# Performance work log

Hardware: AMD Instinct MI355X
Metric: run time of the kernel (lower is better)

Reference implementation:

```python
import jax, jax.numpy as jnp
import numpy as np

B, IN, H, T = 512, 256, 128, 100

def _build_norm_adj():
    # Hardcoded topology from GraphConvLSTM.build_graph (22 nodes, cliques per sublist)
    adj_list = [[0, 2, 5, 8, 11], [0, 1, 4, 7, 10], [0, 3, 6, 9, 12, 15],
                [9, 14, 17, 19, 21], [9, 13, 16, 18, 20]]
    n = max(max(s) for s in adj_list) + 1  # 22
    A = np.zeros((n, n), dtype=np.float32)
    for s in adj_list:
        for i in range(len(s)):
            for j in range(i + 1, len(s)):
                A[s[i], s[j]] = 1.0
                A[s[j], s[i]] = 1.0
    # DGL GraphConv norm='both': D^{-1/2} A D^{-1/2} (degrees clamped to >=1)
    deg = np.clip(A.sum(axis=1), 1.0, None)
    dinv = 1.0 / np.sqrt(deg)
    return jnp.asarray(dinv[:, None] * A * dinv[None, :])  # (N, N)

A_NORM = _build_norm_adj()
N = A_NORM.shape[0]  # 22

def setup_inputs() -> dict:
    key = jax.random.key(0)
    ks = jax.random.split(key, 11)
    s_in = 1.0 / np.sqrt(IN)
    s_h = 1.0 / np.sqrt(H)
    return {
        "x":     jax.random.normal(ks[0], (B, IN), jnp.float32),
        "wi_w":  jax.random.normal(ks[1], (H, IN), jnp.float32) * s_in,
        "wi_b":  jax.random.normal(ks[2], (H,), jnp.float32) * s_in,
        "wf_w":  jax.random.normal(ks[3], (H, IN), jnp.float32) * s_in,
        "wf_b":  jax.random.normal(ks[4], (H,), jnp.float32) * s_in,
        "wo_w":  jax.random.normal(ks[5], (H, IN), jnp.float32) * s_in,
        "wo_b":  jax.random.normal(ks[6], (H,), jnp.float32) * s_in,
        "wc_w":  jax.random.normal(ks[7], (H, IN), jnp.float32) * s_in,
        "wc_b":  jax.random.normal(ks[8], (H,), jnp.float32) * s_in,
        "gcn_w": jax.random.normal(ks[9], (H, H), jnp.float32) * s_h,
        "gcn_b": jax.random.normal(ks[10], (H,), jnp.float32) * s_h,
    }

def reference(x, wi_w, wi_b, wf_w, wf_b, wo_w, wo_b, wc_w, wc_b, gcn_w, gcn_b):
    # x is fixed across timesteps in the original forward -> project gates once.
    xi = (x @ wi_w.T + wi_b)[:, None, :]  # (B,1,H) broadcast over nodes
    xf = (x @ wf_w.T + wf_b)[:, None, :]
    xo = (x @ wo_w.T + wo_b)[:, None, :]
    xc = (x @ wc_w.T + wc_b)[:, None, :]

    def step(carry, _):
        h, c = carry
        # All four gates share the identical gcn_h(g, h_prev) result.
        msg = jnp.einsum('mn,bnh->bmh', A_NORM, h)  # (B,N,H)
        g = msg @ gcn_w + gcn_b
        i_t = jax.nn.sigmoid(xi + g)
        f_t = jax.nn.sigmoid(xf + g)
        o_t = jax.nn.sigmoid(xo + g)
        c_til = jnp.tanh(xc + g)
        c_t = f_t * c + i_t * c_til
        h_t = o_t * jnp.tanh(c_t)
        return (h_t, c_t), h_t

    h0 = jnp.zeros((B, N, H), x.dtype)
    c0 = jnp.zeros((B, N, H), x.dtype)
    _, hs = jax.lax.scan(step, (h0, c0), None, length=T)  # (T,B,N,H)
    out = jnp.transpose(hs, (1, 0, 2, 3)).reshape(B, -1)  # (B, T*N*H)
    return out
```

## Files before the change

kernel.cpp:

```cpp
#include <hip/hip_runtime.h>
#include <hip/hip_bf16.h>
#include <math.h>


#define B_   512
#define IN_  256
#define H_   128
#define T_   100
#define N_   22
#define NH   (N_ * H_)
#define TNH  (T_ * NH)
#define HP   136

typedef __attribute__((ext_vector_type(8))) _Float16 half8_t;
typedef __attribute__((ext_vector_type(4))) float f32x4;

__device__ __forceinline__ float sigm(float x) {
    float e = __builtin_exp2f(x * -1.442695041f);
    return __builtin_amdgcn_rcpf(1.0f + e);
}
__device__ __forceinline__ float tanh_f(float x) {
    float a = fabsf(x);
    float e = __builtin_exp2f(a * -2.885390082f);
    float r = (1.0f - e) * __builtin_amdgcn_rcpf(1.0f + e);
    return copysignf(r, x);
}

__global__ void __launch_bounds__(256, 4)
gclstm_kernel(const float* __restrict__ x,
              const float* __restrict__ wi_w, const float* __restrict__ wi_b,
              const float* __restrict__ wf_w, const float* __restrict__ wf_b,
              const float* __restrict__ wo_w, const float* __restrict__ wo_b,
              const float* __restrict__ wc_w, const float* __restrict__ wc_b,
              const float* __restrict__ gcn_w, const float* __restrict__ gcn_b,
              float* __restrict__ out)
{
    __shared__ __align__(16) _Float16 h_hi[32][HP];
    __shared__ __align__(16) _Float16 h_lo[32][HP];
    __shared__ __align__(16) float hw_lds[N_][H_ + 1];
    __shared__ float xp_lds[4][H_];
    __shared__ __align__(16) float xrow[IN_];

    const int t    = threadIdx.x;
    const int b    = blockIdx.x;
    const int ho   = t & (H_ - 1);
    const int mg   = t >> 7;
    const int wid  = t >> 6;
    const int lane = t & 63;
    const int lrow = lane & 15;
    const int lkg  = lane >> 4;

    if (t < IN_ / 4) {
        reinterpret_cast<float4*>(xrow)[t] =
            reinterpret_cast<const float4*>(x + (size_t)b * IN_)[t];
    }
    for (int e = t; e < 32 * HP / 2; e += 256) ((int*)h_hi)[e] = 0;
    for (int e = t; e < 32 * HP / 2; e += 256) ((int*)h_lo)[e] = 0;
    __syncthreads();

    {
        const float* wA = mg ? wf_w : wi_w;  const float* bA = mg ? wf_b : wi_b;
        const float* wB = mg ? wc_w : wo_w;  const float* bB = mg ? wc_b : wo_b;
        const float* rA = wA + (size_t)ho * IN_;
        const float* rB = wB + (size_t)ho * IN_;
        float accA = bA[ho], accB = bB[ho];
        #pragma unroll
        for (int k4 = 0; k4 < IN_ / 4; ++k4) {
            float4 xv = reinterpret_cast<const float4*>(xrow)[k4];
            float4 wv = reinterpret_cast<const float4*>(rA)[k4];
            accA += wv.x * xv.x + wv.y * xv.y + wv.z * xv.z + wv.w * xv.w;
            float4 uv = reinterpret_cast<const float4*>(rB)[k4];
            accB += uv.x * xv.x + uv.y * xv.y + uv.z * xv.z + uv.w * xv.w;
        }
        xp_lds[mg][ho]     = accA;
        xp_lds[mg + 2][ho] = accB;
    }

    half8_t Wf[2][4];
    #pragma unroll
    for (int tn = 0; tn < 2; ++tn) {
        #pragma unroll
        for (int ks = 0; ks < 4; ++ks) {
            #pragma unroll
            for (int i = 0; i < 8; ++i) {
                const int k   = 32 * ks + 8 * lkg + i;
                const int col = 32 * wid + 16 * tn + lrow;
                Wf[tn][ks][i] = (_Float16)gcn_w[k * H_ + col];
            }
        }
    }
    __syncthreads();

    const float gb   = gcn_b[ho];
    const float xi_r = xp_lds[0][ho] + gb;
    const float xf_r = xp_lds[1][ho] + gb;
    const float xo_r = xp_lds[2][ho] + gb;
    const float xc_r = xp_lds[3][ho] + gb;

    float c_reg[11];
    #pragma unroll
    for (int i = 0; i < 11; ++i) c_reg[i] = 0.0f;

    float* outb = out + (size_t)b * TNH + ho;

    #define D13 0.2773500981126146f
    #define D5  0.4472135954999579f
    #define D4  0.5f
    const float DINV[22] = {D13, D4, D4, D5, D4, D4, D5, D4, D4, D13, D4,
                            D4,  D5, D4, D4, D5, D4, D4, D4, D4, D4,  D4};

    for (int step = 0; step < T_; ++step) {
        f32x4 acc[2][2];
        #pragma unroll
        for (int tm = 0; tm < 2; ++tm)
            #pragma unroll
            for (int tn = 0; tn < 2; ++tn)
                acc[tm][tn] = (f32x4)(0.0f);

        #pragma unroll
        for (int ks = 0; ks < 4; ++ks) {
            const int ko = 32 * ks + 8 * lkg;
            const half8_t Ah0 = *reinterpret_cast<const half8_t*>(&h_hi[lrow][ko]);
            const half8_t Ah1 = *reinterpret_cast<const half8_t*>(&h_hi[16 + lrow][ko]);
            const half8_t Al0 = *reinterpret_cast<const half8_t*>(&h_lo[lrow][ko]);
            const half8_t Al1 = *reinterpret_cast<const half8_t*>(&h_lo[16 + lrow][ko]);
            #pragma unroll
            for (int tn = 0; tn < 2; ++tn) {
                acc[0][tn] = __builtin_amdgcn_mfma_f32_16x16x32_f16(Ah0, Wf[tn][ks], acc[0][tn], 0, 0, 0);
                acc[0][tn] = __builtin_amdgcn_mfma_f32_16x16x32_f16(Al0, Wf[tn][ks], acc[0][tn], 0, 0, 0);
                acc[1][tn] = __builtin_amdgcn_mfma_f32_16x16x32_f16(Ah1, Wf[tn][ks], acc[1][tn], 0, 0, 0);
                acc[1][tn] = __builtin_amdgcn_mfma_f32_16x16x32_f16(Al1, Wf[tn][ks], acc[1][tn], 0, 0, 0);
            }
        }
        #pragma unroll
        for (int tm = 0; tm < 2; ++tm) {
            #pragma unroll
            for (int i = 0; i < 4; ++i) {
                const int row = 16 * tm + 4 * lkg + i;
                if (row < N_) {
                    hw_lds[row][32 * wid + lrow]      = acc[tm][0][i];
                    hw_lds[row][32 * wid + 16 + lrow] = acc[tm][1][i];
                }
            }
        }
        __syncthreads();

        float tt[22];
        #pragma unroll
        for (int m = 0; m < 22; ++m) tt[m] = DINV[m] * hw_lds[m][ho];

        const float S0 = tt[0] + tt[2] + tt[5] + tt[8] + tt[11];
        const float S1 = tt[0] + tt[1] + tt[4] + tt[7] + tt[10];
        const float S2 = tt[0] + tt[3] + tt[6] + tt[9] + tt[12] + tt[15];
        const float S3 = tt[9] + tt[14] + tt[17] + tt[19] + tt[21];
        const float S4 = tt[9] + tt[13] + tt[16] + tt[18] + tt[20];

        float* outs = outb + (size_t)step * NH;

        #define UPD(n, nn, SSexpr, KK) {                                        \
            const float g  = DINV[n] * ((SSexpr) - (KK) * tt[n]);               \
            const float it = sigm(xi_r + g);                                    \
            const float ft = sigm(xf_r + g);                                    \
            const float ot = sigm(xo_r + g);                                    \
            const float ct = tanh_f(xc_r + g);                                  \
            const float cn = ft * c_reg[nn] + it * ct;                          \
            c_reg[nn] = cn;                                                     \
            const float hn = ot * tanh_f(cn);                                   \
            outs[(n) * H_] = hn;                                                \
            const _Float16 hh = (_Float16)hn;                                   \
            h_hi[n][ho] = hh;                                                   \
            h_lo[n][ho] = (_Float16)(hn - (float)hh);                           \
        }

        if (mg == 0) {
            UPD(0, 0, S0 + S1 + S2, 3.0f)
            UPD(1, 1, S1, 1.0f)
            UPD(2, 2, S0, 1.0f)
            UPD(3, 3, S2, 1.0f)
            UPD(4, 4, S1, 1.0f)
            UPD(5, 5, S0, 1.0f)
            UPD(6, 6, S2, 1.0f)
            UPD(7, 7, S1, 1.0f)
            UPD(8, 8, S0, 1.0f)
            UPD(9, 9, S2 + S3 + S4, 3.0f)
            UPD(10, 10, S1, 1.0f)
        } else {
            UPD(11, 0, S0, 1.0f)
            UPD(12, 1, S2, 1.0f)
            UPD(13, 2, S4, 1.0f)
            UPD(14, 3, S3, 1.0f)
            UPD(15, 4, S2, 1.0f)
            UPD(16, 5, S4, 1.0f)
            UPD(17, 6, S3, 1.0f)
            UPD(18, 7, S4, 1.0f)
            UPD(19, 8, S3, 1.0f)
            UPD(20, 9, S4, 1.0f)
            UPD(21, 10, S3, 1.0f)
        }
        #undef UPD
        __syncthreads();
    }
}

extern "C" void kernel_launch(void* const* d_in, const int* in_sizes, int n_in,
                              void* d_out, int out_size, void* d_ws, size_t ws_size,
                              hipStream_t stream) {
    const float* x     = (const float*)d_in[0];
    const float* wi_w  = (const float*)d_in[1];
    const float* wi_b  = (const float*)d_in[2];
    const float* wf_w  = (const float*)d_in[3];
    const float* wf_b  = (const float*)d_in[4];
    const float* wo_w  = (const float*)d_in[5];
    const float* wo_b  = (const float*)d_in[6];
    const float* wc_w  = (const float*)d_in[7];
    const float* wc_b  = (const float*)d_in[8];
    const float* gcn_w = (const float*)d_in[9];
    const float* gcn_b = (const float*)d_in[10];
    float* out = (float*)d_out;

    gclstm_kernel<<<dim3(B_), dim3(256), 0, stream>>>(
        x, wi_w, wi_b, wf_w, wf_b, wo_w, wo_b, wc_w, wc_b, gcn_w, gcn_b, out);
}
```

Measured before the change: 885.0 us.

## Double block size to 512 threads, splitting nodes and MFMA columns across more warps

Each block now has 512 threads (8 warps). Each warp computes a 16-column slice of the h@W product, and the elementwise LSTM node updates are split over four thread groups of 5-6 nodes instead of two groups of 11. The input projection gives one gate per thread group. This is meant to shorten the serial per-step critical path by using more parallel lanes per batch element, at the cost of fewer resident blocks per CU and more threads taking part in each barrier.

New measurement: 902.1 us. About the same (+1.9%).

```diff
diff --git a/kernel.cpp b/kernel.cpp
--- a/kernel.cpp
+++ b/kernel.cpp
@@ -11,6 +11,7 @@
 #define NH   (N_ * H_)
 #define TNH  (T_ * NH)
 #define HP   136
+#define THREADS 512
 
 typedef __attribute__((ext_vector_type(8))) _Float16 half8_t;
 typedef __attribute__((ext_vector_type(4))) float f32x4;
@@ -26,7 +27,7 @@
     return copysignf(r, x);
 }
 
-__global__ void __launch_bounds__(256, 4)
+__global__ void __launch_bounds__(THREADS, 4)
 gclstm_kernel(const float* __restrict__ x,
               const float* __restrict__ wi_w, const float* __restrict__ wi_b,
               const float* __restrict__ wf_w, const float* __restrict__ wf_b,
@@ -54,39 +55,32 @@
         reinterpret_cast<float4*>(xrow)[t] =
             reinterpret_cast<const float4*>(x + (size_t)b * IN_)[t];
     }
-    for (int e = t; e < 32 * HP / 2; e += 256) ((int*)h_hi)[e] = 0;
-    for (int e = t; e < 32 * HP / 2; e += 256) ((int*)h_lo)[e] = 0;
+    for (int e = t; e < 32 * HP / 2; e += THREADS) ((int*)h_hi)[e] = 0;
+    for (int e = t; e < 32 * HP / 2; e += THREADS) ((int*)h_lo)[e] = 0;
     __syncthreads();
 
     {
-        const float* wA = mg ? wf_w : wi_w;  const float* bA = mg ? wf_b : wi_b;
-        const float* wB = mg ? wc_w : wo_w;  const float* bB = mg ? wc_b : wo_b;
-        const float* rA = wA + (size_t)ho * IN_;
-        const float* rB = wB + (size_t)ho * IN_;
-        float accA = bA[ho], accB = bB[ho];
+        const float* wg = (mg == 0) ? wi_w : (mg == 1) ? wf_w : (mg == 2) ? wo_w : wc_w;
+        const float* bg = (mg == 0) ? wi_b : (mg == 1) ? wf_b : (mg == 2) ? wo_b : wc_b;
+        const float* rg = wg + (size_t)ho * IN_;
+        float acc = bg[ho];
         #pragma unroll
         for (int k4 = 0; k4 < IN_ / 4; ++k4) {
             float4 xv = reinterpret_cast<const float4*>(xrow)[k4];
-            float4 wv = reinterpret_cast<const float4*>(rA)[k4];
-            accA += wv.x * xv.x + wv.y * xv.y + wv.z * xv.z + wv.w * xv.w;
-            float4 uv = reinterpret_cast<const float4*>(rB)[k4];
-            accB += uv.x * xv.x + uv.y * xv.y + uv.z * xv.z + uv.w * xv.w;
-        }
-        xp_lds[mg][ho]     = accA;
-        xp_lds[mg + 2][ho] = accB;
-    }
-
-    half8_t Wf[2][4];
+            float4 wv = reinterpret_cast<const float4*>(rg)[k4];
+            acc += wv.x * xv.x + wv.y * xv.y + wv.z * xv.z + wv.w * xv.w;
+        }
+        xp_lds[mg][ho] = acc;
+    }
+
+    half8_t Wf[4];
     #pragma unroll
-    for (int tn = 0; tn < 2; ++tn) {
-        #pragma unroll
-        for (int ks = 0; ks < 4; ++ks) {
-            #pragma unroll
-            for (int i = 0; i < 8; ++i) {
-                const int k   = 32 * ks + 8 * lkg + i;
-                const int col = 32 * wid + 16 * tn + lrow;
-                Wf[tn][ks][i] = (_Float16)gcn_w[k * H_ + col];
-            }
+    for (int ks = 0; ks < 4; ++ks) {
+        #pragma unroll
+        for (int i = 0; i < 8; ++i) {
+            const int k   = 32 * ks + 8 * lkg + i;
+            const int col = 16 * wid + lrow;
+            Wf[ks][i] = (_Float16)gcn_w[k * H_ + col];
         }
     }
     __syncthreads();
@@ -97,9 +91,9 @@
     const float xo_r = xp_lds[2][ho] + gb;
     const float xc_r = xp_lds[3][ho] + gb;
 
-    float c_reg[11];
+    float c_reg[6];
     #pragma unroll
-    for (int i = 0; i < 11; ++i) c_reg[i] = 0.0f;
+    for (int i = 0; i < 6; ++i) c_reg[i] = 0.0f;
 
     float* outb = out + (size_t)b * TNH + ho;
 
@@ -110,12 +104,8 @@
                             D4,  D5, D4, D4, D5, D4, D4, D4, D4, D4,  D4};
 
     for (int step = 0; step < T_; ++step) {
-        f32x4 acc[2][2];
-        #pragma unroll
-        for (int tm = 0; tm < 2; ++tm)
-            #pragma unroll
-            for (int tn = 0; tn < 2; ++tn)
-                acc[tm][tn] = (f32x4)(0.0f);
+        f32x4 acc0 = (f32x4)(0.0f);
+        f32x4 acc1 = (f32x4)(0.0f);
 
         #pragma unroll
         for (int ks = 0; ks < 4; ++ks) {
@@ -124,24 +114,17 @@
             const half8_t Ah1 = *reinterpret_cast<const half8_t*>(&h_hi[16 + lrow][ko]);
             const half8_t Al0 = *reinterpret_cast<const half8_t*>(&h_lo[lrow][ko]);
             const half8_t Al1 = *reinterpret_cast<const half8_t*>(&h_lo[16 + lrow][ko]);
-            #pragma unroll
-            for (int tn = 0; tn < 2; ++tn) {
-                acc[0][tn] = __builtin_amdgcn_mfma_f32_16x16x32_f16(Ah0, Wf[tn][ks], acc[0][tn], 0, 0, 0);
-                acc[0][tn] = __builtin_amdgcn_mfma_f32_16x16x32_f16(Al0, Wf[tn][ks], acc[0][tn], 0, 0, 0);
-                acc[1][tn] = __builtin_amdgcn_mfma_f32_16x16x32_f16(Ah1, Wf[tn][ks], acc[1][tn], 0, 0, 0);
-                acc[1][tn] = __builtin_amdgcn_mfma_f32_16x16x32_f16(Al1, Wf[tn][ks], acc[1][tn], 0, 0, 0);
-            }
-        }
-        #pragma unroll
-        for (int tm = 0; tm < 2; ++tm) {
-            #pragma unroll
-            for (int i = 0; i < 4; ++i) {
-                const int row = 16 * tm + 4 * lkg + i;
-                if (row < N_) {
-                    hw_lds[row][32 * wid + lrow]      = acc[tm][0][i];
-                    hw_lds[row][32 * wid + 16 + lrow] = acc[tm][1][i];
-                }
-            }
+            acc0 = __builtin_amdgcn_mfma_f32_16x16x32_f16(Ah0, Wf[ks], acc0, 0, 0, 0);
+            acc0 = __builtin_amdgcn_mfma_f32_16x16x32_f16(Al0, Wf[ks], acc0, 0, 0, 0);
+            acc1 = __builtin_amdgcn_mfma_f32_16x16x32_f16(Ah1, Wf[ks], acc1, 0, 0, 0);
+            acc1 = __builtin_amdgcn_mfma_f32_16x16x32_f16(Al1, Wf[ks], acc1, 0, 0, 0);
+        }
+        #pragma unroll
+        for (int i = 0; i < 4; ++i) {
+            const int row = 4 * lkg + i;
+            hw_lds[row][16 * wid + lrow] = acc0[i];
+            const int row2 = 16 + row;
+            if (row2 < N_) hw_lds[row2][16 * wid + lrow] = acc1[i];
         }
         __syncthreads();
 
@@ -179,23 +162,25 @@
             UPD(3, 3, S2, 1.0f)
             UPD(4, 4, S1, 1.0f)
             UPD(5, 5, S0, 1.0f)
-            UPD(6, 6, S2, 1.0f)
-            UPD(7, 7, S1, 1.0f)
-            UPD(8, 8, S0, 1.0f)
-            UPD(9, 9, S2 + S3 + S4, 3.0f)
-            UPD(10, 10, S1, 1.0f)
-        } else {
+        } else if (mg == 1) {
+            UPD(6, 0, S2, 1.0f)
+            UPD(7, 1, S1, 1.0f)
+            UPD(8, 2, S0, 1.0f)
+            UPD(9, 3, S2 + S3 + S4, 3.0f)
+            UPD(10, 4, S1, 1.0f)
+        } else if (mg == 2) {
             UPD(11, 0, S0, 1.0f)
             UPD(12, 1, S2, 1.0f)
             UPD(13, 2, S4, 1.0f)
             UPD(14, 3, S3, 1.0f)
             UPD(15, 4, S2, 1.0f)
             UPD(16, 5, S4, 1.0f)
-            UPD(17, 6, S3, 1.0f)
-            UPD(18, 7, S4, 1.0f)
-            UPD(19, 8, S3, 1.0f)
-            UPD(20, 9, S4, 1.0f)
-            UPD(21, 10, S3, 1.0f)
+        } else {
+            UPD(17, 0, S3, 1.0f)
+            UPD(18, 1, S4, 1.0f)
+            UPD(19, 2, S3, 1.0f)
+            UPD(20, 3, S4, 1.0f)
+            UPD(21, 4, S3, 1.0f)
         }
         #undef UPD
         __syncthreads();
@@ -218,6 +203,6 @@
     const float* gcn_b = (const float*)d_in[10];
     float* out = (float*)d_out;
 
-    gclstm_kernel<<<dim3(B_), dim3(256), 0, stream>>>(
+    gclstm_kernel<<<dim3(B_), dim3(THREADS), 0, stream>>>(
         x, wi_w, wi_b, wf_w, wf_b, wo_w, wo_b, wc_w, wc_b, gcn_w, gcn_b, out);
 }
```
